# Kernel optimization log

Hardware: AMD Instinct MI355X
Metric: run time of the kernel (lower is better)

The kernel has to match this reference:

```python
import jax, jax.numpy as jnp
import numpy as np

B, T, C, H = 4, 2048, 512, 8
D = C // H  # dim_per_head = 64


def setup_inputs() -> dict:
    key = jax.random.key(0)
    ks = jax.random.split(key, 16)
    s = 1.0 / np.sqrt(C)
    return {
        "query": jax.random.normal(ks[0], (B, T, C), jnp.float32),
        "key": jax.random.normal(ks[1], (B, T, C), jnp.float32),
        "value": jax.random.normal(ks[2], (B, T, C), jnp.float32),
        "pos_embed": jax.random.normal(ks[3], (B, T, C), jnp.float32),
        "Wq": jax.random.normal(ks[4], (C, C), jnp.float32) * s,
        "bq": jnp.zeros((C,), jnp.float32),
        "Wk": jax.random.normal(ks[5], (C, C), jnp.float32) * s,
        "bk": jnp.zeros((C,), jnp.float32),
        "Wv": jax.random.normal(ks[6], (C, C), jnp.float32) * s,
        "bv": jnp.zeros((C,), jnp.float32),
        "Wpos": jax.random.normal(ks[7], (C, C), jnp.float32) * s,
        "pos_bias_u": jax.random.normal(ks[8], (H, D), jnp.float32) * 0.1,
        "pos_bias_v": jax.random.normal(ks[9], (H, D), jnp.float32) * 0.1,
        "Wo": jax.random.normal(ks[10], (C, C), jnp.float32) * s,
        "bo": jnp.zeros((C,), jnp.float32),
    }


def _relative_shift(pos_score):
    # pos_score: [B, H, T1, T2] -- Transformer-XL style shift
    b, h, t1, t2 = pos_score.shape
    padded = jnp.pad(pos_score, ((0, 0), (0, 0), (0, 0), (1, 0)))  # [B,H,T1,T2+1]
    padded = padded.reshape(b, h, t2 + 1, t1)
    return padded[:, :, 1:].reshape(b, h, t1, t2)


def reference(query, key, value, pos_embed, Wq, bq, Wk, bk, Wv, bv, Wpos,
              pos_bias_u, pos_bias_v, Wo, bo):
    q = (query @ Wq + bq).reshape(B, T, H, D)                    # b l h d
    k = (key @ Wk + bk).reshape(B, T, H, D)                      # b l h d
    v = (value @ Wv + bv).reshape(B, T, H, D)
    p = (pos_embed @ Wpos).reshape(B, T, H, D)
    # content score: (q + u) k^T ; pos score: (q + v) p^T
    content = jnp.einsum('bihd,bjhd->bhij', q + pos_bias_u, k)
    pos = jnp.einsum('bihd,bjhd->bhij', q + pos_bias_v, p)
    pos = _relative_shift(pos)
    scores = (content + pos) / jnp.sqrt(jnp.float32(D))
    attn = jax.nn.softmax(scores, axis=-1)
    ctx = jnp.einsum('bhij,bjhd->bihd', attn, v).reshape(B, T, C)
    return ctx @ Wo + bo
```

## Files before the change

### kernel.cpp

```cpp
#include <hip/hip_runtime.h>


#define Bb 4
#define Tt 2048
#define Cc 512
#define Hh 8
#define Dd 64

typedef __bf16 bf16_t;
typedef __bf16 bf16x8 __attribute__((ext_vector_type(8)));
typedef __bf16 bf16x4 __attribute__((ext_vector_type(4)));
typedef float  f32x4  __attribute__((ext_vector_type(4)));

__global__ __launch_bounds__(256, 4)
void wsplit_kernel(const float* __restrict__ Wq, const float* __restrict__ Wk,
                   const float* __restrict__ Wv, const float* __restrict__ Wp,
                   const float* __restrict__ Wo,
                   bf16_t* __restrict__ WT4, bf16_t* __restrict__ WoT, int mode)
{
    const int w = (mode < 0) ? (int)blockIdx.y : 4;
    const float* W = (w == 0) ? Wq : (w == 1) ? Wk : (w == 2) ? Wv : (w == 3) ? Wp : Wo;
    bf16_t* dh = (w == 4) ? WoT : WT4 + (size_t)w * 2 * 262144;
    bf16_t* dl = dh + 262144;

    const int tile = blockIdx.x;
    const int k0 = (tile >> 3) * 64;
    const int n0 = (tile & 7) * 64;
    const int tid = threadIdx.x;

    __shared__ bf16_t th[64][66];
    __shared__ bf16_t tl[64][66];

#pragma unroll
    for (int rep = 0; rep < 4; rep++) {
        int id = rep * 256 + tid;
        int kk = id >> 4, ns = id & 15;
        f32x4 v = *(const f32x4*)&W[(size_t)(k0 + kk) * 512 + n0 + ns * 4];
#pragma unroll
        for (int e = 0; e < 4; e++) {
            bf16_t h = (bf16_t)v[e];
            th[kk][ns * 4 + e] = h;
            tl[kk][ns * 4 + e] = (bf16_t)(v[e] - (float)h);
        }
    }
    __syncthreads();
#pragma unroll
    for (int rep = 0; rep < 2; rep++) {
        int id = rep * 256 + tid;
        int nn = id >> 3, ks = id & 7;
        bf16x8 hv, lv;
#pragma unroll
        for (int j = 0; j < 8; j++) { hv[j] = th[ks * 8 + j][nn]; lv[j] = tl[ks * 8 + j][nn]; }
        *(bf16x8*)&dh[(size_t)(n0 + nn) * 512 + k0 + ks * 8] = hv;
        *(bf16x8*)&dl[(size_t)(n0 + nn) * 512 + k0 + ks * 8] = lv;
    }
}

__global__ __launch_bounds__(256, 3)
void split_gemm_kernel(const float* __restrict__ Xq, const float* __restrict__ Xk,
                       const float* __restrict__ Xv, const float* __restrict__ Xp,
                       const bf16_t* __restrict__ WT4,
                       const float* __restrict__ bq, const float* __restrict__ bk,
                       const float* __restrict__ bv,
                       const float* __restrict__ bias_u, const float* __restrict__ bias_v,
                       bf16_t* __restrict__ QU, bf16_t* __restrict__ QV,
                       bf16_t* __restrict__ K16, bf16_t* __restrict__ VT16,
                       bf16_t* __restrict__ P16)
{
    const int z = blockIdx.z;
    const float* X    = (z == 0) ? Xq : (z == 1) ? Xk : (z == 2) ? Xv : Xp;
    const bf16_t* Wh  = WT4 + (size_t)z * 2 * 262144;
    const bf16_t* Wl  = Wh + 262144;
    const float* bias = (z == 0) ? bq : (z == 1) ? bk : (z == 2) ? bv : nullptr;

    const int bx = blockIdx.x;
    const int g  = bx >> 3, x8 = bx & 7;
    const int mtile = (g >> 2) * 8 + x8;
    const int ntile = g & 3;
    const int r0 = mtile * 128;
    const int c0 = ntile * 128;

    const int tid  = threadIdx.x;
    const int wave = tid >> 6;
    const int lane = tid & 63;
    const int quad = lane >> 4;
    const int l16  = lane & 15;
    const int rb = (wave >> 1) * 64;
    const int cb = (wave & 1) * 64;

    __shared__ __align__(16) bf16_t Ah[128][40];
    __shared__ __align__(16) bf16_t Al[128][40];
    __shared__ __align__(16) bf16_t Bh[128][40];
    __shared__ __align__(16) bf16_t Bl[128][40];

    f32x4 acc[4][4];
#pragma unroll
    for (int mt = 0; mt < 4; mt++)
#pragma unroll
        for (int nt = 0; nt < 4; nt++)
#pragma unroll
            for (int r = 0; r < 4; r++) acc[mt][nt][r] = 0.f;

    f32x4  xa[4];
    bf16x8 wbh[2], wbl[2];

#pragma unroll
    for (int rep = 0; rep < 4; rep++) {
        int id = rep * 256 + tid;
        int m = id >> 3, c = id & 7;
        xa[rep] = *(const f32x4*)&X[(size_t)(r0 + m) * 512 + c * 4];
    }
#pragma unroll
    for (int rep = 0; rep < 2; rep++) {
        int id = rep * 256 + tid;
        int n = id >> 2, seg = id & 3;
        wbh[rep] = *(const bf16x8*)&Wh[(size_t)(c0 + n) * 512 + seg * 8];
        wbl[rep] = *(const bf16x8*)&Wl[(size_t)(c0 + n) * 512 + seg * 8];
    }

    for (int it = 0; it < 16; ++it) {
#pragma unroll
        for (int rep = 0; rep < 4; rep++) {
            int id = rep * 256 + tid;
            int m = id >> 3, c = id & 7;
            f32x4 v = xa[rep];
            bf16x4 hh, ll;
#pragma unroll
            for (int e = 0; e < 4; e++) {
                bf16_t hv = (bf16_t)v[e];
                hh[e] = hv;
                ll[e] = (bf16_t)(v[e] - (float)hv);
            }
            *(bf16x4*)&Ah[m][c * 4] = hh;
            *(bf16x4*)&Al[m][c * 4] = ll;
        }
#pragma unroll
        for (int rep = 0; rep < 2; rep++) {
            int id = rep * 256 + tid;
            int n = id >> 2, seg = id & 3;
            *(bf16x8*)&Bh[n][seg * 8] = wbh[rep];
            *(bf16x8*)&Bl[n][seg * 8] = wbl[rep];
        }
        __syncthreads();

        if (it < 15) {
            const int k0n = (it + 1) * 32;
#pragma unroll
            for (int rep = 0; rep < 4; rep++) {
                int id = rep * 256 + tid;
                int m = id >> 3, c = id & 7;
                xa[rep] = *(const f32x4*)&X[(size_t)(r0 + m) * 512 + k0n + c * 4];
            }
#pragma unroll
            for (int rep = 0; rep < 2; rep++) {
                int id = rep * 256 + tid;
                int n = id >> 2, seg = id & 3;
                wbh[rep] = *(const bf16x8*)&Wh[(size_t)(c0 + n) * 512 + k0n + seg * 8];
                wbl[rep] = *(const bf16x8*)&Wl[(size_t)(c0 + n) * 512 + k0n + seg * 8];
            }
        }

        {
            bf16x8 bh[4], bl[4], ah[4], al[4];
#pragma unroll
            for (int nt = 0; nt < 4; nt++) {
                bh[nt] = *(const bf16x8*)&Bh[cb + nt * 16 + l16][quad * 8];
                bl[nt] = *(const bf16x8*)&Bl[cb + nt * 16 + l16][quad * 8];
            }
#pragma unroll
            for (int mt = 0; mt < 4; mt++) {
                ah[mt] = *(const bf16x8*)&Ah[rb + mt * 16 + l16][quad * 8];
                al[mt] = *(const bf16x8*)&Al[rb + mt * 16 + l16][quad * 8];
            }
#pragma unroll
            for (int mt = 0; mt < 4; mt++) {
#pragma unroll
                for (int nt = 0; nt < 4; nt++) {
                    acc[mt][nt] = __builtin_amdgcn_mfma_f32_16x16x32_bf16(ah[mt], bh[nt], acc[mt][nt], 0, 0, 0);
                    acc[mt][nt] = __builtin_amdgcn_mfma_f32_16x16x32_bf16(ah[mt], bl[nt], acc[mt][nt], 0, 0, 0);
                    acc[mt][nt] = __builtin_amdgcn_mfma_f32_16x16x32_bf16(al[mt], bh[nt], acc[mt][nt], 0, 0, 0);
                }
            }
        }
        __syncthreads();
    }

#pragma unroll
    for (int mt = 0; mt < 4; mt++) {
#pragma unroll
        for (int r = 0; r < 4; r++) {
            int row = r0 + rb + mt * 16 + quad * 4 + r;
#pragma unroll
            for (int nt = 0; nt < 4; nt++) {
                int col = c0 + cb + nt * 16 + l16;
                float y = acc[mt][nt][r] + (bias ? bias[col] : 0.f);
                int b = row >> 11, t = row & 2047;
                int h = col >> 6,  d = col & 63;
                if (z == 0) {
                    size_t idx = (((size_t)(b * Hh + h)) * Tt + t) * Dd + d;
                    QU[idx] = (bf16_t)(y + bias_u[col]);
                    QV[idx] = (bf16_t)(y + bias_v[col]);
                } else if (z == 1) {
                    size_t idx = (((size_t)(b * Hh + h)) * Tt + t) * Dd + d;
                    K16[idx] = (bf16_t)y;
                } else if (z == 2) {
                    size_t idx = (((size_t)(b * Hh + h)) * Dd + d) * Tt + t;
                    VT16[idx] = (bf16_t)y;
                } else {
                    size_t idx = (((size_t)(b * Hh + h)) * Tt + t) * Dd + d;
                    P16[idx] = (bf16_t)y;
                }
            }
        }
    }
}

__global__ __launch_bounds__(256, 4)
void out_gemm_kernel(const float* __restrict__ Xc, const bf16_t* __restrict__ WoT,
                     const float* __restrict__ bo, float* __restrict__ OUT)
{
    const bf16_t* Wh = WoT;
    const bf16_t* Wl = WoT + 262144;

    const int bx = blockIdx.x;
    const int r0 = (bx >> 2) * 64;
    const int c0 = (bx & 3) * 128;

    const int tid  = threadIdx.x;
    const int wave = tid >> 6;
    const int lane = tid & 63;
    const int quad = lane >> 4;
    const int l16  = lane & 15;
    const int rb = (wave >> 1) * 32;
    const int cb = (wave & 1) * 64;

    __shared__ __align__(16) bf16_t Ah[64][40];
    __shared__ __align__(16) bf16_t Al[64][40];
    __shared__ __align__(16) bf16_t Bh[128][40];
    __shared__ __align__(16) bf16_t Bl[128][40];

    f32x4 acc[2][4];
#pragma unroll
    for (int mt = 0; mt < 2; mt++)
#pragma unroll
        for (int nt = 0; nt < 4; nt++)
#pragma unroll
            for (int r = 0; r < 4; r++) acc[mt][nt][r] = 0.f;

    f32x4  xa[2];
    bf16x8 wbh[2], wbl[2];

#pragma unroll
    for (int rep = 0; rep < 2; rep++) {
        int id = rep * 256 + tid;
        int m = id >> 3, c = id & 7;
        xa[rep] = *(const f32x4*)&Xc[(size_t)(r0 + m) * 512 + c * 4];
    }
#pragma unroll
    for (int rep = 0; rep < 2; rep++) {
        int id = rep * 256 + tid;
        int n = id >> 2, seg = id & 3;
        wbh[rep] = *(const bf16x8*)&Wh[(size_t)(c0 + n) * 512 + seg * 8];
        wbl[rep] = *(const bf16x8*)&Wl[(size_t)(c0 + n) * 512 + seg * 8];
    }

    for (int it = 0; it < 16; ++it) {
#pragma unroll
        for (int rep = 0; rep < 2; rep++) {
            int id = rep * 256 + tid;
            int m = id >> 3, c = id & 7;
            f32x4 v = xa[rep];
            bf16x4 hh, ll;
#pragma unroll
            for (int e = 0; e < 4; e++) {
                bf16_t hv = (bf16_t)v[e];
                hh[e] = hv;
                ll[e] = (bf16_t)(v[e] - (float)hv);
            }
            *(bf16x4*)&Ah[m][c * 4] = hh;
            *(bf16x4*)&Al[m][c * 4] = ll;
        }
#pragma unroll
        for (int rep = 0; rep < 2; rep++) {
            int id = rep * 256 + tid;
            int n = id >> 2, seg = id & 3;
            *(bf16x8*)&Bh[n][seg * 8] = wbh[rep];
            *(bf16x8*)&Bl[n][seg * 8] = wbl[rep];
        }
        __syncthreads();

        if (it < 15) {
            const int k0n = (it + 1) * 32;
#pragma unroll
            for (int rep = 0; rep < 2; rep++) {
                int id = rep * 256 + tid;
                int m = id >> 3, c = id & 7;
                xa[rep] = *(const f32x4*)&Xc[(size_t)(r0 + m) * 512 + k0n + c * 4];
            }
#pragma unroll
            for (int rep = 0; rep < 2; rep++) {
                int id = rep * 256 + tid;
                int n = id >> 2, seg = id & 3;
                wbh[rep] = *(const bf16x8*)&Wh[(size_t)(c0 + n) * 512 + k0n + seg * 8];
                wbl[rep] = *(const bf16x8*)&Wl[(size_t)(c0 + n) * 512 + k0n + seg * 8];
            }
        }

        {
            bf16x8 bh[4], bl[4], ah[2], al[2];
#pragma unroll
            for (int nt = 0; nt < 4; nt++) {
                bh[nt] = *(const bf16x8*)&Bh[cb + nt * 16 + l16][quad * 8];
                bl[nt] = *(const bf16x8*)&Bl[cb + nt * 16 + l16][quad * 8];
            }
#pragma unroll
            for (int mt = 0; mt < 2; mt++) {
                ah[mt] = *(const bf16x8*)&Ah[rb + mt * 16 + l16][quad * 8];
                al[mt] = *(const bf16x8*)&Al[rb + mt * 16 + l16][quad * 8];
            }
#pragma unroll
            for (int mt = 0; mt < 2; mt++) {
#pragma unroll
                for (int nt = 0; nt < 4; nt++) {
                    acc[mt][nt] = __builtin_amdgcn_mfma_f32_16x16x32_bf16(ah[mt], bh[nt], acc[mt][nt], 0, 0, 0);
                    acc[mt][nt] = __builtin_amdgcn_mfma_f32_16x16x32_bf16(ah[mt], bl[nt], acc[mt][nt], 0, 0, 0);
                    acc[mt][nt] = __builtin_amdgcn_mfma_f32_16x16x32_bf16(al[mt], bh[nt], acc[mt][nt], 0, 0, 0);
                }
            }
        }
        __syncthreads();
    }

#pragma unroll
    for (int mt = 0; mt < 2; mt++) {
#pragma unroll
        for (int r = 0; r < 4; r++) {
            int row = r0 + rb + mt * 16 + quad * 4 + r;
#pragma unroll
            for (int nt = 0; nt < 4; nt++) {
                int col = c0 + cb + nt * 16 + l16;
                OUT[(size_t)row * 512 + col] = acc[mt][nt][r] + bo[col];
            }
        }
    }
}

struct Band { int d_hi, w1, prow1, w2, e_lo, c2_0, nct1, nct2; };

__device__ __forceinline__ Band mkband(int i0, int j0)
{
    Band b;
    int d_lo = i0 - (j0 + 63);
    b.d_hi = i0 + 63 - j0;
    b.w1 = 0; b.prow1 = 0;
    if (b.d_hi >= 0) {
        int b1 = d_lo > 0 ? d_lo : 0;
        b.w1 = b.d_hi - b1 + 1;
        b.prow1 = (Tt - 1) - b.d_hi;
    }
    int dmax2 = b.d_hi < -2 ? b.d_hi : -2;
    b.w2 = 0; b.e_lo = 0;
    if (d_lo <= dmax2) {
        b.e_lo = -dmax2 - 2;
        int e_hi = -d_lo - 2;
        b.w2 = e_hi - b.e_lo + 1;
    }
    b.c2_0 = b.d_hi + 2 + b.e_lo;
    b.nct1 = (b.w1 + 15) >> 4;
    b.nct2 = (b.w2 + 15) >> 4;
    return b;
}

__global__ __launch_bounds__(256, 4)
void attn_kernel(const bf16_t* __restrict__ QU, const bf16_t* __restrict__ QV,
                 const bf16_t* __restrict__ K16, const bf16_t* __restrict__ VT16,
                 const bf16_t* __restrict__ P16, float* __restrict__ CTX)
{
    const int bh = blockIdx.x;
    const int i0 = blockIdx.y * 64;
    const int b = bh >> 3, h = bh & 7;
    const int tid = threadIdx.x;
    const int wave = tid >> 6;
    const int lane = tid & 63;
    const int quad = lane >> 4;
    const int l16 = lane & 15;

    const bf16_t* qu_g = QU + (size_t)bh * Tt * Dd;
    const bf16_t* qv_g = QV + (size_t)bh * Tt * Dd;
    const bf16_t* k_g  = K16 + (size_t)bh * Tt * Dd;
    const bf16_t* vt_g = VT16 + (size_t)bh * Dd * Tt;
    const bf16_t* p_g  = P16 + (size_t)bh * Tt * Dd;

    __shared__ __align__(16) char smem[38912];
    bf16_t (*pA)[72]  = (bf16_t (*)[72])(smem);
    bf16_t (*k_s)[72] = (bf16_t (*)[72])(smem + 18432);
    bf16_t (*msw)[88] = (bf16_t (*)[88])(smem + 27648);

    const int off_w = 48 - wave * 16;
    const int cmin = 48 - wave * 16;
    const int cmax = 126 - wave * 16;

    const int srow = tid >> 3;
    const int sseg = tid & 7;

    const int qrow = i0 + wave * 16 + l16;
    const int qrow2 = (qrow + 1 > Tt - 1) ? (Tt - 1) : (qrow + 1);
    bf16x8 aq[2], av1[2], av2[2];
#pragma unroll
    for (int kc = 0; kc < 2; kc++) {
        aq[kc]  = *(const bf16x8*)(qu_g + (size_t)qrow  * Dd + kc * 32 + quad * 8);
        av1[kc] = *(const bf16x8*)(qv_g + (size_t)qrow  * Dd + kc * 32 + quad * 8);
        av2[kc] = *(const bf16x8*)(qv_g + (size_t)qrow2 * Dd + kc * 32 + quad * 8);
    }

    float lsum[4];
    f32x4 accO[4];
#pragma unroll
    for (int r = 0; r < 4; r++) lsum[r] = 0.f;
#pragma unroll
    for (int dt = 0; dt < 4; dt++)
#pragma unroll
        for (int r = 0; r < 4; r++) accO[dt][r] = 0.f;

    f32x4 kr0, kr1, pr0, pr1, pr2, pr3;
    Band bp = mkband(i0, 0);
    {
        kr0 = *(const f32x4*)(k_g + (size_t)(0 + srow) * Dd + sseg * 8);
        kr1 = *(const f32x4*)(k_g + (size_t)(0 + srow + 32) * Dd + sseg * 8);
        int r0_ = srow,      s0 = (r0_ < bp.w1) ? bp.prow1 + r0_ : bp.e_lo + r0_ - bp.w1;
        int r1_ = srow + 32, s1 = (r1_ < bp.w1) ? bp.prow1 + r1_ : bp.e_lo + r1_ - bp.w1;
        int r2_ = srow + 64, s2 = (r2_ < bp.w1) ? bp.prow1 + r2_ : bp.e_lo + r2_ - bp.w1;
        int r3_ = srow + 96, s3 = (r3_ < bp.w1) ? bp.prow1 + r3_ : bp.e_lo + r3_ - bp.w1;
        if (s0 > Tt - 1) s0 = Tt - 1;
        if (s1 > Tt - 1) s1 = Tt - 1;
        if (s2 > Tt - 1) s2 = Tt - 1;
        if (s3 > Tt - 1) s3 = Tt - 1;
        pr0 = *(const f32x4*)(p_g + (size_t)s0 * Dd + sseg * 8);
        pr1 = *(const f32x4*)(p_g + (size_t)s1 * Dd + sseg * 8);
        pr2 = *(const f32x4*)(p_g + (size_t)s2 * Dd + sseg * 8);
        pr3 = *(const f32x4*)(p_g + (size_t)s3 * Dd + sseg * 8);
    }

    for (int j0 = 0; j0 < Tt; j0 += 64) {
        const Band bc = bp;

        *(f32x4*)&k_s[srow][sseg * 8]      = kr0;
        *(f32x4*)&k_s[srow + 32][sseg * 8] = kr1;
        {
            int wtot = bc.w1 + bc.w2;
            if (srow < wtot)      *(f32x4*)&pA[srow][sseg * 8]      = pr0;
            if (srow + 32 < wtot) *(f32x4*)&pA[srow + 32][sseg * 8] = pr1;
            if (srow + 64 < wtot) *(f32x4*)&pA[srow + 64][sseg * 8] = pr2;
            if (srow + 96 < wtot) *(f32x4*)&pA[srow + 96][sseg * 8] = pr3;
        }
        __syncthreads();

        if (j0 + 64 < Tt) {
            bp = mkband(i0, j0 + 64);
            kr0 = *(const f32x4*)(k_g + (size_t)(j0 + 64 + srow) * Dd + sseg * 8);
            kr1 = *(const f32x4*)(k_g + (size_t)(j0 + 64 + srow + 32) * Dd + sseg * 8);
            int r0_ = srow,      s0 = (r0_ < bp.w1) ? bp.prow1 + r0_ : bp.e_lo + r0_ - bp.w1;
            int r1_ = srow + 32, s1 = (r1_ < bp.w1) ? bp.prow1 + r1_ : bp.e_lo + r1_ - bp.w1;
            int r2_ = srow + 64, s2 = (r2_ < bp.w1) ? bp.prow1 + r2_ : bp.e_lo + r2_ - bp.w1;
            int r3_ = srow + 96, s3 = (r3_ < bp.w1) ? bp.prow1 + r3_ : bp.e_lo + r3_ - bp.w1;
            if (s0 > Tt - 1) s0 = Tt - 1;
            if (s1 > Tt - 1) s1 = Tt - 1;
            if (s2 > Tt - 1) s2 = Tt - 1;
            if (s3 > Tt - 1) s3 = Tt - 1;
            pr0 = *(const f32x4*)(p_g + (size_t)s0 * Dd + sseg * 8);
            pr1 = *(const f32x4*)(p_g + (size_t)s1 * Dd + sseg * 8);
            pr2 = *(const f32x4*)(p_g + (size_t)s2 * Dd + sseg * 8);
            pr3 = *(const f32x4*)(p_g + (size_t)s3 * Dd + sseg * 8);
        }

        f32x4 accS[4];
#pragma unroll
        for (int nt = 0; nt < 4; nt++) {
            f32x4 acc = {0.f, 0.f, 0.f, 0.f};
#pragma unroll
            for (int kc = 0; kc < 2; kc++) {
                bf16x8 bk8 = *(const bf16x8*)&k_s[nt * 16 + l16][kc * 32 + quad * 8];
                acc = __builtin_amdgcn_mfma_f32_16x16x32_bf16(aq[kc], bk8, acc, 0, 0, 0);
            }
            accS[nt] = acc;
        }

        for (int ct = 0; ct < bc.nct1 + bc.nct2; ct++) {
            bool b2 = ct >= bc.nct1;
            int rb_ = b2 ? (bc.w1 + (ct - bc.nct1) * 16) : (ct * 16);
            int cb_ = b2 ? (bc.c2_0 + (ct - bc.nct1) * 16) : (ct * 16);
            if (cb_ > cmax || cb_ + 15 < cmin) continue;
            f32x4 acc = {0.f, 0.f, 0.f, 0.f};
#pragma unroll
            for (int kc = 0; kc < 2; kc++) {
                bf16x8 bp8 = *(const bf16x8*)&pA[rb_ + l16][kc * 32 + quad * 8];
                acc = b2 ? __builtin_amdgcn_mfma_f32_16x16x32_bf16(av2[kc], bp8, acc, 0, 0, 0)
                         : __builtin_amdgcn_mfma_f32_16x16x32_bf16(av1[kc], bp8, acc, 0, 0, 0);
            }
            int colp = cb_ + l16 - off_w;
            if ((unsigned)colp < 80u) {
#pragma unroll
                for (int r = 0; r < 4; r++)
                    msw[wave * 16 + quad * 4 + r][colp] = (bf16_t)acc[r];
            }
        }
        {
            int zcl = bc.d_hi + 1 - off_w;
            if ((unsigned)zcl < 80u && quad == 0)
                msw[wave * 16 + l16][zcl] = (bf16_t)0.f;
        }

        float wv[4][4];
#pragma unroll
        for (int nt = 0; nt < 4; nt++) {
#pragma unroll
            for (int r = 0; r < 4; r++) {
                float pos = (float)msw[wave * 16 + quad * 4 + r]
                                    [nt * 16 + l16 + 15 - (quad * 4 + r)];
                float x = accS[nt][r] + pos;
                float a = fminf(fmaf(x, 0.18033688f, -17.3123405f), 120.0f);
                float w = exp2f(a);
                lsum[r] += w;
                wv[nt][r] = w;
            }
        }
#pragma unroll
        for (int nt = 0; nt < 4; nt++)
#pragma unroll
            for (int r = 0; r < 4; r++)
                msw[wave * 16 + quad * 4 + r][nt * 16 + l16] = (bf16_t)wv[nt][r];

#pragma unroll
        for (int kc = 0; kc < 2; kc++) {
            bf16x8 aw = *(const bf16x8*)&msw[wave * 16 + l16][kc * 32 + quad * 8];
#pragma unroll
            for (int dt = 0; dt < 4; dt++) {
                bf16x8 bv8 = *(const bf16x8*)(vt_g + (size_t)(dt * 16 + l16) * Tt + j0 + kc * 32 + quad * 8);
                accO[dt] = __builtin_amdgcn_mfma_f32_16x16x32_bf16(aw, bv8, accO[dt], 0, 0, 0);
            }
        }
        __syncthreads();
    }

#pragma unroll
    for (int r = 0; r < 4; r++) {
#pragma unroll
        for (int off = 1; off < 16; off <<= 1) lsum[r] += __shfl_xor(lsum[r], off, 64);
    }

#pragma unroll
    for (int r = 0; r < 4; r++) {
        int il = wave * 16 + quad * 4 + r;
        int ig = i0 + il;
        float inv = 1.0f / lsum[r];
#pragma unroll
        for (int dt = 0; dt < 4; dt++) {
            CTX[((size_t)(b * Tt + ig)) * Cc + h * Dd + dt * 16 + l16] = accO[dt][r] * inv;
        }
    }
}

extern "C" void kernel_launch(void* const* d_in, const int* in_sizes, int n_in,
                              void* d_out, int out_size, void* d_ws, size_t ws_size,
                              hipStream_t stream)
{
    const float* query = (const float*)d_in[0];
    const float* key   = (const float*)d_in[1];
    const float* value = (const float*)d_in[2];
    const float* pemb  = (const float*)d_in[3];
    const float* Wq    = (const float*)d_in[4];
    const float* bq    = (const float*)d_in[5];
    const float* Wk    = (const float*)d_in[6];
    const float* bk    = (const float*)d_in[7];
    const float* Wv    = (const float*)d_in[8];
    const float* bv    = (const float*)d_in[9];
    const float* Wpos  = (const float*)d_in[10];
    const float* pbu   = (const float*)d_in[11];
    const float* pbv   = (const float*)d_in[12];
    const float* Wo    = (const float*)d_in[13];
    const float* bo    = (const float*)d_in[14];

    const size_t NE = (size_t)Bb * Hh * Tt * Dd;
    bf16_t* QU   = (bf16_t*)d_ws;
    bf16_t* QV   = QU + NE;
    bf16_t* K16  = QV + NE;
    bf16_t* VT16 = K16 + NE;
    bf16_t* P16  = VT16 + NE;
    float*  CTX  = (float*)(P16 + NE);

    bf16_t* WT4 = (bf16_t*)CTX;
    bf16_t* WoT = (bf16_t*)QU;

    wsplit_kernel<<<dim3(64, 4), 256, 0, stream>>>(Wq, Wk, Wv, Wpos, Wo, WT4, WoT, -1);

    split_gemm_kernel<<<dim3(256, 1, 4), 256, 0, stream>>>(
        query, key, value, pemb, WT4,
        bq, bk, bv, pbu, pbv, QU, QV, K16, VT16, P16);

    attn_kernel<<<dim3(32, 32), 256, 0, stream>>>(QU, QV, K16, VT16, P16, CTX);

    wsplit_kernel<<<dim3(64, 1), 256, 0, stream>>>(Wq, Wk, Wv, Wpos, Wo, WT4, WoT, 4);

    out_gemm_kernel<<<dim3(512), 256, 0, stream>>>(CTX, WoT, bo, (float*)d_out);
}
```

Baseline: 411.3 us.

## Stream weight tiles directly into double-buffered LDS via global_load_lds

In the projection and output GEMM kernels, the bf16 weight tiles are now loaded straight from global memory into shared memory with global_load_lds. The B tiles are double-buffered, and LDS padding is removed (row stride 40 becomes 32). This is meant to drop the register staging and the ds_write instructions for the weights and overlap their loads with compute. In exchange it removes the padding that avoided bank conflicts on the MFMA fragment reads. The direct-to-LDS loads also rely on the existing barriers for ordering, which is a correctness risk since no explicit vmcnt wait is visible.

```diff
diff --git a/kernel.cpp b/kernel.cpp
--- a/kernel.cpp
+++ b/kernel.cpp
@@ -11,6 +11,11 @@
 typedef __bf16 bf16x8 __attribute__((ext_vector_type(8)));
 typedef __bf16 bf16x4 __attribute__((ext_vector_type(4)));
 typedef float  f32x4  __attribute__((ext_vector_type(4)));
+
+__device__ __forceinline__ void gload16(const bf16_t* g, bf16_t* l)
+{
+    __builtin_amdgcn_global_load_lds(g, l, 16, 0, 0);
+}
 
 __global__ __launch_bounds__(256, 4)
 void wsplit_kernel(const float* __restrict__ Wq, const float* __restrict__ Wk,
@@ -88,10 +93,10 @@
     const int rb = (wave >> 1) * 64;
     const int cb = (wave & 1) * 64;
 
-    __shared__ __align__(16) bf16_t Ah[128][40];
-    __shared__ __align__(16) bf16_t Al[128][40];
-    __shared__ __align__(16) bf16_t Bh[128][40];
-    __shared__ __align__(16) bf16_t Bl[128][40];
+    __shared__ __align__(16) bf16_t Ah[128][32];
+    __shared__ __align__(16) bf16_t Al[128][32];
+    __shared__ __align__(16) bf16_t Bh[2][128][32];
+    __shared__ __align__(16) bf16_t Bl[2][128][32];
 
     f32x4 acc[4][4];
 #pragma unroll
@@ -101,28 +106,25 @@
 #pragma unroll
             for (int r = 0; r < 4; r++) acc[mt][nt][r] = 0.f;
 
-    f32x4  xa[4];
-    bf16x8 wbh[2], wbl[2];
-
-#pragma unroll
-    for (int rep = 0; rep < 4; rep++) {
-        int id = rep * 256 + tid;
-        int m = id >> 3, c = id & 7;
-        xa[rep] = *(const f32x4*)&X[(size_t)(r0 + m) * 512 + c * 4];
-    }
+    const int am = tid >> 3, ac = tid & 7;
+    const int brow = tid >> 2, bseg = tid & 3;
+
+    f32x4 xa[4];
+
+#pragma unroll
+    for (int rep = 0; rep < 4; rep++)
+        xa[rep] = *(const f32x4*)&X[(size_t)(r0 + am + rep * 32) * 512 + ac * 4];
 #pragma unroll
     for (int rep = 0; rep < 2; rep++) {
-        int id = rep * 256 + tid;
-        int n = id >> 2, seg = id & 3;
-        wbh[rep] = *(const bf16x8*)&Wh[(size_t)(c0 + n) * 512 + seg * 8];
-        wbl[rep] = *(const bf16x8*)&Wl[(size_t)(c0 + n) * 512 + seg * 8];
+        gload16(&Wh[(size_t)(c0 + rep * 64 + brow) * 512 + bseg * 8],
+                &Bh[0][rep * 64 + brow][bseg * 8]);
+        gload16(&Wl[(size_t)(c0 + rep * 64 + brow) * 512 + bseg * 8],
+                &Bl[0][rep * 64 + brow][bseg * 8]);
     }
 
     for (int it = 0; it < 16; ++it) {
 #pragma unroll
         for (int rep = 0; rep < 4; rep++) {
-            int id = rep * 256 + tid;
-            int m = id >> 3, c = id & 7;
             f32x4 v = xa[rep];
             bf16x4 hh, ll;
 #pragma unroll
@@ -131,41 +133,33 @@
                 hh[e] = hv;
                 ll[e] = (bf16_t)(v[e] - (float)hv);
             }
-            *(bf16x4*)&Ah[m][c * 4] = hh;
-            *(bf16x4*)&Al[m][c * 4] = ll;
-        }
-#pragma unroll
-        for (int rep = 0; rep < 2; rep++) {
-            int id = rep * 256 + tid;
-            int n = id >> 2, seg = id & 3;
-            *(bf16x8*)&Bh[n][seg * 8] = wbh[rep];
-            *(bf16x8*)&Bl[n][seg * 8] = wbl[rep];
+            *(bf16x4*)&Ah[am + rep * 32][ac * 4] = hh;
+            *(bf16x4*)&Al[am + rep * 32][ac * 4] = ll;
         }
         __syncthreads();
 
         if (it < 15) {
             const int k0n = (it + 1) * 32;
-#pragma unroll
-            for (int rep = 0; rep < 4; rep++) {
-                int id = rep * 256 + tid;
-                int m = id >> 3, c = id & 7;
-                xa[rep] = *(const f32x4*)&X[(size_t)(r0 + m) * 512 + k0n + c * 4];
-            }
+            const int nb = (it + 1) & 1;
 #pragma unroll
             for (int rep = 0; rep < 2; rep++) {
-                int id = rep * 256 + tid;
-                int n = id >> 2, seg = id & 3;
-                wbh[rep] = *(const bf16x8*)&Wh[(size_t)(c0 + n) * 512 + k0n + seg * 8];
-                wbl[rep] = *(const bf16x8*)&Wl[(size_t)(c0 + n) * 512 + k0n + seg * 8];
-            }
+                gload16(&Wh[(size_t)(c0 + rep * 64 + brow) * 512 + k0n + bseg * 8],
+                        &Bh[nb][rep * 64 + brow][bseg * 8]);
+                gload16(&Wl[(size_t)(c0 + rep * 64 + brow) * 512 + k0n + bseg * 8],
+                        &Bl[nb][rep * 64 + brow][bseg * 8]);
+            }
+#pragma unroll
+            for (int rep = 0; rep < 4; rep++)
+                xa[rep] = *(const f32x4*)&X[(size_t)(r0 + am + rep * 32) * 512 + k0n + ac * 4];
         }
 
         {
+            const int cbuf = it & 1;
             bf16x8 bh[4], bl[4], ah[4], al[4];
 #pragma unroll
             for (int nt = 0; nt < 4; nt++) {
-                bh[nt] = *(const bf16x8*)&Bh[cb + nt * 16 + l16][quad * 8];
-                bl[nt] = *(const bf16x8*)&Bl[cb + nt * 16 + l16][quad * 8];
+                bh[nt] = *(const bf16x8*)&Bh[cbuf][cb + nt * 16 + l16][quad * 8];
+                bl[nt] = *(const bf16x8*)&Bl[cbuf][cb + nt * 16 + l16][quad * 8];
             }
 #pragma unroll
             for (int mt = 0; mt < 4; mt++) {
@@ -234,10 +228,10 @@
     const int rb = (wave >> 1) * 32;
     const int cb = (wave & 1) * 64;
 
-    __shared__ __align__(16) bf16_t Ah[64][40];
-    __shared__ __align__(16) bf16_t Al[64][40];
-    __shared__ __align__(16) bf16_t Bh[128][40];
-    __shared__ __align__(16) bf16_t Bl[128][40];
+    __shared__ __align__(16) bf16_t Ah[64][32];
+    __shared__ __align__(16) bf16_t Al[64][32];
+    __shared__ __align__(16) bf16_t Bh[2][128][32];
+    __shared__ __align__(16) bf16_t Bl[2][128][32];
 
     f32x4 acc[2][4];
 #pragma unroll
@@ -247,28 +241,25 @@
 #pragma unroll
             for (int r = 0; r < 4; r++) acc[mt][nt][r] = 0.f;
 
-    f32x4  xa[2];
-    bf16x8 wbh[2], wbl[2];
-
+    const int am = tid >> 3, ac = tid & 7;
+    const int brow = tid >> 2, bseg = tid & 3;
+
+    f32x4 xa[2];
+
+#pragma unroll
+    for (int rep = 0; rep < 2; rep++)
+        xa[rep] = *(const f32x4*)&Xc[(size_t)(r0 + am + rep * 32) * 512 + ac * 4];
 #pragma unroll
     for (int rep = 0; rep < 2; rep++) {
-        int id = rep * 256 + tid;
-        int m = id >> 3, c = id & 7;
-        xa[rep] = *(const f32x4*)&Xc[(size_t)(r0 + m) * 512 + c * 4];
-    }
-#pragma unroll
-    for (int rep = 0; rep < 2; rep++) {
-        int id = rep * 256 + tid;
-        int n = id >> 2, seg = id & 3;
-        wbh[rep] = *(const bf16x8*)&Wh[(size_t)(c0 + n) * 512 + seg * 8];
-        wbl[rep] = *(const bf16x8*)&Wl[(size_t)(c0 + n) * 512 + seg * 8];
+        gload16(&Wh[(size_t)(c0 + rep * 64 + brow) * 512 + bseg * 8],
+                &Bh[0][rep * 64 + brow][bseg * 8]);
+        gload16(&Wl[(size_t)(c0 + rep * 64 + brow) * 512 + bseg * 8],
+                &Bl[0][rep * 64 + brow][bseg * 8]);
     }
 
     for (int it = 0; it < 16; ++it) {
 #pragma unroll
         for (int rep = 0; rep < 2; rep++) {
-            int id = rep * 256 + tid;
-            int m = id >> 3, c = id & 7;
             f32x4 v = xa[rep];
             bf16x4 hh, ll;
 #pragma unroll
@@ -277,41 +268,33 @@
                 hh[e] = hv;
                 ll[e] = (bf16_t)(v[e] - (float)hv);
             }
-            *(bf16x4*)&Ah[m][c * 4] = hh;
-            *(bf16x4*)&Al[m][c * 4] = ll;
-        }
-#pragma unroll
-        for (int rep = 0; rep < 2; rep++) {
-            int id = rep * 256 + tid;
-            int n = id >> 2, seg = id & 3;
-            *(bf16x8*)&Bh[n][seg * 8] = wbh[rep];
-            *(bf16x8*)&Bl[n][seg * 8] = wbl[rep];
+            *(bf16x4*)&Ah[am + rep * 32][ac * 4] = hh;
+            *(bf16x4*)&Al[am + rep * 32][ac * 4] = ll;
         }
         __syncthreads();
 
         if (it < 15) {
             const int k0n = (it + 1) * 32;
+            const int nb = (it + 1) & 1;
 #pragma unroll
             for (int rep = 0; rep < 2; rep++) {
-                int id = rep * 256 + tid;
-                int m = id >> 3, c = id & 7;
-                xa[rep] = *(const f32x4*)&Xc[(size_t)(r0 + m) * 512 + k0n + c * 4];
-            }
-#pragma unroll
-            for (int rep = 0; rep < 2; rep++) {
-                int id = rep * 256 + tid;
-                int n = id >> 2, seg = id & 3;
-                wbh[rep] = *(const bf16x8*)&Wh[(size_t)(c0 + n) * 512 + k0n + seg * 8];
-                wbl[rep] = *(const bf16x8*)&Wl[(size_t)(c0 + n) * 512 + k0n + seg * 8];
-            }
+                gload16(&Wh[(size_t)(c0 + rep * 64 + brow) * 512 + k0n + bseg * 8],
+                        &Bh[nb][rep * 64 + brow][bseg * 8]);
+                gload16(&Wl[(size_t)(c0 + rep * 64 + brow) * 512 + k0n + bseg * 8],
+                        &Bl[nb][rep * 64 + brow][bseg * 8]);
+            }
+#pragma unroll
+            for (int rep = 0; rep < 2; rep++)
+                xa[rep] = *(const f32x4*)&Xc[(size_t)(r0 + am + rep * 32) * 512 + k0n + ac * 4];
         }
 
         {
+            const int cbuf = it & 1;
             bf16x8 bh[4], bl[4], ah[2], al[2];
 #pragma unroll
             for (int nt = 0; nt < 4; nt++) {
-                bh[nt] = *(const bf16x8*)&Bh[cb + nt * 16 + l16][quad * 8];
-                bl[nt] = *(const bf16x8*)&Bl[cb + nt * 16 + l16][quad * 8];
+                bh[nt] = *(const bf16x8*)&Bh[cbuf][cb + nt * 16 + l16][quad * 8];
+                bl[nt] = *(const bf16x8*)&Bl[cbuf][cb + nt * 16 + l16][quad * 8];
             }
 #pragma unroll
             for (int mt = 0; mt < 2; mt++) {
```

Result: no change. 408.1 us (-0.8%).
